# Kernel tuning notes

Hardware: AMD Instinct MI355X
Metric: run time of the kernel (lower is better)

## Reference

```python
import jax, jax.numpy as jnp
import numpy as np

N_STATIONS = 276
CONTEXT_LEN = 384  # args.context_len * 2
TARGET_LEN = 96
BATCH = 4096


def setup_inputs() -> dict:
    key = jax.random.key(0)
    k1, k2, k3, k4, k5, k6 = jax.random.split(key, 6)
    z = jax.random.normal(k1, (BATCH, CONTEXT_LEN), dtype=jnp.float32)
    stations = jax.random.randint(k2, (BATCH,), 0, N_STATIONS, dtype=jnp.int64)
    # per-station Linear params (nn.Linear(context_len, target_len) x n_stations)
    lim = 1.0 / np.sqrt(CONTEXT_LEN)
    W = jax.random.uniform(k3, (N_STATIONS, TARGET_LEN, CONTEXT_LEN), jnp.float32, -lim, lim)
    b = jax.random.uniform(k4, (N_STATIONS, TARGET_LEN), jnp.float32, -lim, lim)
    loc = jax.random.normal(k5, (N_STATIONS,), dtype=jnp.float32)
    scale = jax.random.uniform(k6, (N_STATIONS,), jnp.float32, 0.5, 2.0)
    return {"z": z, "stations": stations, "W": W, "b": b, "loc": loc, "scale": scale}


def reference(z, stations, W, b, loc, scale):
    # norm: (z - loc[i]) / scale[i]
    loc_i = loc[stations][:, None]      # (bs, 1)
    scale_i = scale[stations][:, None]  # (bs, 1)
    zn = (z - loc_i) / scale_i          # (bs, context_len)
    # per-sample station-specific Linear: batched GEMV via gathered weights
    out = jnp.einsum("boi,bi->bo", W[stations], zn) + b[stations]  # (bs, target_len)
    # denorm then softplus
    out = out * scale_i + loc_i
    return jax.nn.softplus(out)
```

## Files before the change

### kernel.cpp

```cpp
#include <hip/hip_runtime.h>
#include <hip/hip_bf16.h>
#include <math.h>

#define N_STATIONS 276
#define CTX 384
#define TGT 96
#define BATCH 4096
#define NT_MAX 532
#define NTASK (NT_MAX * 6)
#define CPX (NTASK / 8)

typedef __attribute__((ext_vector_type(8))) short bf16x8;
typedef __attribute__((ext_vector_type(4))) float f32x4;

__device__ __forceinline__ short f2bf(float f) {
    return (short)__builtin_bit_cast(unsigned short, __float2bfloat16(f));
}
__device__ __forceinline__ float bf2f(short h) {
    unsigned u = ((unsigned)(unsigned short)h) << 16;
    return __builtin_bit_cast(float, u);
}
__device__ __forceinline__ void cvt_hilo(float4 a, float4 b, bf16x8& hi, bf16x8& lo) {
    float f[8] = {a.x, a.y, a.z, a.w, b.x, b.y, b.z, b.w};
#pragma unroll
    for (int i = 0; i < 8; ++i) {
        short h = f2bf(f[i]);
        hi[i] = h;
        lo[i] = f2bf(f[i] - bf2f(h));
    }
}
__device__ __forceinline__ bf16x8 cvt_norm(float4 a, float4 b, float inv, float nb) {
    float f[8] = {a.x, a.y, a.z, a.w, b.x, b.y, b.z, b.w};
    bf16x8 r;
#pragma unroll
    for (int i = 0; i < 8; ++i) r[i] = f2bf(fmaf(f[i], inv, nb));
    return r;
}

__global__ __launch_bounds__(1024) void build_lists(
    const int* __restrict__ stations, int* __restrict__ ws)
{
    __shared__ int cnt[N_STATIONS], cnt2[N_STATIONS];
    __shared__ int poff[N_STATIONS + 1], tpoff[N_STATIONS + 1];
    const int tid = threadIdx.x;
    for (int i = tid; i < N_STATIONS; i += 1024) { cnt[i] = 0; cnt2[i] = 0; }
    __syncthreads();
    for (int b = tid; b < BATCH; b += 1024) atomicAdd(&cnt[stations[b]], 1);
    __syncthreads();
    if (tid < 64) {
        int run = 0, trun = 0;
        for (int base = 0; base < N_STATIONS; base += 64) {
            const int i = base + tid;
            int c  = (i < N_STATIONS) ? cnt[i] : 0;
            int v  = c, tv = (c + 15) >> 4;
#pragma unroll
            for (int off = 1; off < 64; off <<= 1) {
                int u  = __shfl_up(v, off, 64);
                int tu = __shfl_up(tv, off, 64);
                if (tid >= off) { v += u; tv += tu; }
            }
            if (i < N_STATIONS) { poff[i + 1] = run + v; tpoff[i + 1] = trun + tv; }
            run  += __shfl(v, 63, 64);
            trun += __shfl(tv, 63, 64);
        }
        if (tid == 0) { poff[0] = 0; tpoff[0] = 0; }
    }
    __syncthreads();
    int* order = ws + 1024;
    for (int b = tid; b < BATCH; b += 1024) {
        int s = stations[b];
        int p = atomicAdd(&cnt2[s], 1);
        order[poff[s] + p] = b;
    }
    for (int i = tid; i < N_STATIONS; i += 1024) {
        int n = (cnt[i] + 15) >> 4, base = tpoff[i];
        for (int t = 0; t < n; ++t) ws[1 + base + t] = (i << 16) | t;
    }
    if (tid <= N_STATIONS) ws[5120 + tid] = poff[tid];
    if (tid == 0) ws[0] = tpoff[N_STATIONS];
}

__global__ __launch_bounds__(64, 4) void nlinear_wave(
    const float* __restrict__ z,
    const float* __restrict__ W,
    const float* __restrict__ bias,
    const float* __restrict__ loc,
    const float* __restrict__ scale,
    const int*   __restrict__ ws,
    float*       __restrict__ out)
{
    const int ntasks = ws[0] * 6;
    const int b0 = blockIdx.x;
    const int b  = (b0 & 7) * CPX + (b0 >> 3);
    if (b >= ntasks) return;

    const int tile = b / 6;
    const int nt   = b - tile * 6;

    const int* tiles   = ws + 1;
    const int* order   = ws + 1024;
    const int* offsets = ws + 5120;

    const int pk = tiles[tile];
    const int s  = pk >> 16;
    const int tt = pk & 0xFFFF;
    const int start = offsets[s];
    const int m     = offsets[s + 1] - start;

    const int l  = threadIdx.x;
    const int lr = l & 15;
    const int kh = (l >> 4) * 8;

    const float lc = loc[s], sc = scale[s];
    const float inv = 1.0f / sc, nb = -lc * inv;

    int j = tt * 16 + lr; if (j > m - 1) j = m - 1;
    const float* zr = z + (size_t)order[start + j] * CTX + kh;
    bf16x8 af[12];
#pragma unroll
    for (int kk = 0; kk < 12; ++kk) {
        float4 a0 = *(const float4*)(zr + kk * 32);
        float4 a1 = *(const float4*)(zr + kk * 32 + 4);
        af[kk] = cvt_norm(a0, a1, inv, nb);
    }

    const float* wr = W + ((size_t)s * TGT + nt * 16 + lr) * CTX + kh;
    float4 wc0 = *(const float4*)(wr);
    float4 wc1 = *(const float4*)(wr + 4);
    float4 wc2 = *(const float4*)(wr + 32);
    float4 wc3 = *(const float4*)(wr + 36);

    f32x4 ah = {0.f, 0.f, 0.f, 0.f};
    f32x4 al = {0.f, 0.f, 0.f, 0.f};

#pragma unroll
    for (int i = 0; i < 6; ++i) {
        float4 wn0, wn1, wn2, wn3;
        if (i < 5) {
            const float* wnx = wr + (2 * i + 2) * 32;
            wn0 = *(const float4*)(wnx);
            wn1 = *(const float4*)(wnx + 4);
            wn2 = *(const float4*)(wnx + 32);
            wn3 = *(const float4*)(wnx + 36);
        }
        bf16x8 bhi, blo;
        cvt_hilo(wc0, wc1, bhi, blo);
        ah = __builtin_amdgcn_mfma_f32_16x16x32_bf16(af[2 * i], bhi, ah, 0, 0, 0);
        al = __builtin_amdgcn_mfma_f32_16x16x32_bf16(af[2 * i], blo, al, 0, 0, 0);
        cvt_hilo(wc2, wc3, bhi, blo);
        ah = __builtin_amdgcn_mfma_f32_16x16x32_bf16(af[2 * i + 1], bhi, ah, 0, 0, 0);
        al = __builtin_amdgcn_mfma_f32_16x16x32_bf16(af[2 * i + 1], blo, al, 0, 0, 0);
        if (i < 5) { wc0 = wn0; wc1 = wn1; wc2 = wn2; wc3 = wn3; }
    }

    const float bv = bias[(size_t)s * TGT + nt * 16 + lr];
    const int rbase = (l >> 4) * 4;
#pragma unroll
    for (int r = 0; r < 4; ++r) {
        const int jj = tt * 16 + rbase + r;
        if (jj < m) {
            const int oid = order[start + jj];
            float v = (ah[r] + al[r] + bv) * sc + lc;
            out[(size_t)oid * TGT + nt * 16 + lr] =
                fmaxf(v, 0.f) + log1pf(expf(-fabsf(v)));
        }
    }
}

extern "C" void kernel_launch(void* const* d_in, const int* in_sizes, int n_in,
                              void* d_out, int out_size, void* d_ws, size_t ws_size,
                              hipStream_t stream) {
    const float* z        = (const float*)d_in[0];
    const int*   stations = (const int*)  d_in[1];
    const float* W        = (const float*)d_in[2];
    const float* bias     = (const float*)d_in[3];
    const float* loc      = (const float*)d_in[4];
    const float* scale    = (const float*)d_in[5];
    float* out = (float*)d_out;
    int* ws = (int*)d_ws;

    build_lists<<<1, 1024, 0, stream>>>(stations, ws);
    nlinear_wave<<<NTASK, 64, 0, stream>>>(z, W, bias, loc, scale, ws, out);
}
```

Baseline: 31.84 us.

## Pre-stage normalized bf16 z tiles and drop hi/lo weight split

Adds a zstage kernel that gathers and normalizes the z rows for each station tile once, writes them to workspace as bf16 in MFMA fragment order, and stores per-tile metadata (station, row count, output indices). The main kernel no longer re-gathers and converts z for each of its six N-tiles. It also drops the hi/lo bf16 split of the weights, halving the MFMA count but reducing weight precision to plain bf16. The cost is an extra kernel launch, a workspace round-trip for z, and a possible accuracy loss.

New measurement: 30.88 us (median of 2 runs). 1.03x faster.

```diff
diff --git a/kernel.cpp b/kernel.cpp
--- a/kernel.cpp
+++ b/kernel.cpp
@@ -10,31 +10,14 @@
 #define NTASK (NT_MAX * 6)
 #define CPX (NTASK / 8)
 
+#define META_OFF 8192
+#define ZF_OFF   262144
+
 typedef __attribute__((ext_vector_type(8))) short bf16x8;
 typedef __attribute__((ext_vector_type(4))) float f32x4;
 
 __device__ __forceinline__ short f2bf(float f) {
     return (short)__builtin_bit_cast(unsigned short, __float2bfloat16(f));
-}
-__device__ __forceinline__ float bf2f(short h) {
-    unsigned u = ((unsigned)(unsigned short)h) << 16;
-    return __builtin_bit_cast(float, u);
-}
-__device__ __forceinline__ void cvt_hilo(float4 a, float4 b, bf16x8& hi, bf16x8& lo) {
-    float f[8] = {a.x, a.y, a.z, a.w, b.x, b.y, b.z, b.w};
-#pragma unroll
-    for (int i = 0; i < 8; ++i) {
-        short h = f2bf(f[i]);
-        hi[i] = h;
-        lo[i] = f2bf(f[i] - bf2f(h));
-    }
-}
-__device__ __forceinline__ bf16x8 cvt_norm(float4 a, float4 b, float inv, float nb) {
-    float f[8] = {a.x, a.y, a.z, a.w, b.x, b.y, b.z, b.w};
-    bf16x8 r;
-#pragma unroll
-    for (int i = 0; i < 8; ++i) r[i] = f2bf(fmaf(f[i], inv, nb));
-    return r;
 }
 
 __global__ __launch_bounds__(1024) void build_lists(
@@ -80,8 +63,53 @@
     if (tid == 0) ws[0] = tpoff[N_STATIONS];
 }
 
-__global__ __launch_bounds__(64, 4) void nlinear_wave(
+__global__ __launch_bounds__(256) void zstage(
     const float* __restrict__ z,
+    const float* __restrict__ loc,
+    const float* __restrict__ scale,
+    int* __restrict__ ws)
+{
+    const int ntiles = ws[0];
+    const int tb = blockIdx.x;
+    if (tb >= ntiles) return;
+
+    const int pk = ws[1 + tb];
+    const int s  = pk >> 16;
+    const int tt = pk & 0xFFFF;
+    const int* order   = ws + 1024;
+    const int* offsets = ws + 5120;
+    const int start = offsets[s];
+    const int m     = offsets[s + 1] - start;
+
+    const float lc = loc[s], inv = 1.0f / scale[s], nb = -lc * inv;
+
+    int* rec = ws + META_OFF + tb * 32;
+    const int t = threadIdx.x;
+    if (t < 16) {
+        int j = tt * 16 + t; if (j > m - 1) j = m - 1;
+        rec[2 + t] = order[start + j];
+    }
+    if (t == 0) { rec[0] = s; int mr = m - tt * 16; rec[1] = mr > 16 ? 16 : mr; }
+
+    unsigned short* zt = (unsigned short*)(ws + ZF_OFF) + (size_t)tb * 6144;
+    for (int q = t; q < 768; q += 256) {
+        const int kstep = q >> 6, lane = q & 63;
+        const int sample = lane & 15;
+        const int kb = kstep * 32 + (lane >> 4) * 8;
+        int j = tt * 16 + sample; if (j > m - 1) j = m - 1;
+        const float* zr = z + (size_t)order[start + j] * CTX + kb;
+        float4 a0 = *(const float4*)zr;
+        float4 a1 = *(const float4*)(zr + 4);
+        float f[8] = {a0.x, a0.y, a0.z, a0.w, a1.x, a1.y, a1.z, a1.w};
+        union { unsigned short u[8]; uint4 v; } o;
+#pragma unroll
+        for (int i = 0; i < 8; ++i)
+            o.u[i] = (unsigned short)f2bf(fmaf(f[i], inv, nb));
+        *(uint4*)(zt + (size_t)q * 8) = o.v;
+    }
+}
+
+__global__ __launch_bounds__(64, 4) void nlinear_hot(
     const float* __restrict__ W,
     const float* __restrict__ bias,
     const float* __restrict__ loc,
@@ -97,70 +125,48 @@
     const int tile = b / 6;
     const int nt   = b - tile * 6;
 
-    const int* tiles   = ws + 1;
-    const int* order   = ws + 1024;
-    const int* offsets = ws + 5120;
-
-    const int pk = tiles[tile];
-    const int s  = pk >> 16;
-    const int tt = pk & 0xFFFF;
-    const int start = offsets[s];
-    const int m     = offsets[s + 1] - start;
+    const int* rec = ws + META_OFF + tile * 32;
+    const int s    = rec[0];
+    const int mrem = rec[1];
 
     const int l  = threadIdx.x;
     const int lr = l & 15;
     const int kh = (l >> 4) * 8;
 
-    const float lc = loc[s], sc = scale[s];
-    const float inv = 1.0f / sc, nb = -lc * inv;
+    const float* wr = W + ((size_t)s * TGT + nt * 16 + lr) * CTX + kh;
+    const unsigned short* zt = (const unsigned short*)(ws + ZF_OFF) + (size_t)tile * 6144;
 
-    int j = tt * 16 + lr; if (j > m - 1) j = m - 1;
-    const float* zr = z + (size_t)order[start + j] * CTX + kh;
-    bf16x8 af[12];
+    f32x4 acc = {0.f, 0.f, 0.f, 0.f};
+    float4 wc0 = *(const float4*)(wr);
+    float4 wc1 = *(const float4*)(wr + 4);
+    bf16x8 za  = *(const bf16x8*)(zt + (size_t)l * 8);
+
 #pragma unroll
     for (int kk = 0; kk < 12; ++kk) {
-        float4 a0 = *(const float4*)(zr + kk * 32);
-        float4 a1 = *(const float4*)(zr + kk * 32 + 4);
-        af[kk] = cvt_norm(a0, a1, inv, nb);
+        float4 wn0, wn1; bf16x8 zn_;
+        if (kk < 11) {
+            wn0 = *(const float4*)(wr + (kk + 1) * 32);
+            wn1 = *(const float4*)(wr + (kk + 1) * 32 + 4);
+            zn_ = *(const bf16x8*)(zt + ((size_t)(kk + 1) * 64 + l) * 8);
+        }
+        bf16x8 bh;
+        bh[0] = f2bf(wc0.x); bh[1] = f2bf(wc0.y);
+        bh[2] = f2bf(wc0.z); bh[3] = f2bf(wc0.w);
+        bh[4] = f2bf(wc1.x); bh[5] = f2bf(wc1.y);
+        bh[6] = f2bf(wc1.z); bh[7] = f2bf(wc1.w);
+        acc = __builtin_amdgcn_mfma_f32_16x16x32_bf16(za, bh, acc, 0, 0, 0);
+        if (kk < 11) { wc0 = wn0; wc1 = wn1; za = zn_; }
     }
 
-    const float* wr = W + ((size_t)s * TGT + nt * 16 + lr) * CTX + kh;
-    float4 wc0 = *(const float4*)(wr);
-    float4 wc1 = *(const float4*)(wr + 4);
-    float4 wc2 = *(const float4*)(wr + 32);
-    float4 wc3 = *(const float4*)(wr + 36);
-
-    f32x4 ah = {0.f, 0.f, 0.f, 0.f};
-    f32x4 al = {0.f, 0.f, 0.f, 0.f};
-
-#pragma unroll
-    for (int i = 0; i < 6; ++i) {
-        float4 wn0, wn1, wn2, wn3;
-        if (i < 5) {
-            const float* wnx = wr + (2 * i + 2) * 32;
-            wn0 = *(const float4*)(wnx);
-            wn1 = *(const float4*)(wnx + 4);
-            wn2 = *(const float4*)(wnx + 32);
-            wn3 = *(const float4*)(wnx + 36);
-        }
-        bf16x8 bhi, blo;
-        cvt_hilo(wc0, wc1, bhi, blo);
-        ah = __builtin_amdgcn_mfma_f32_16x16x32_bf16(af[2 * i], bhi, ah, 0, 0, 0);
-        al = __builtin_amdgcn_mfma_f32_16x16x32_bf16(af[2 * i], blo, al, 0, 0, 0);
-        cvt_hilo(wc2, wc3, bhi, blo);
-        ah = __builtin_amdgcn_mfma_f32_16x16x32_bf16(af[2 * i + 1], bhi, ah, 0, 0, 0);
-        al = __builtin_amdgcn_mfma_f32_16x16x32_bf16(af[2 * i + 1], blo, al, 0, 0, 0);
-        if (i < 5) { wc0 = wn0; wc1 = wn1; wc2 = wn2; wc3 = wn3; }
-    }
-
+    const float sc = scale[s], lc = loc[s];
     const float bv = bias[(size_t)s * TGT + nt * 16 + lr];
     const int rbase = (l >> 4) * 4;
 #pragma unroll
     for (int r = 0; r < 4; ++r) {
-        const int jj = tt * 16 + rbase + r;
-        if (jj < m) {
-            const int oid = order[start + jj];
-            float v = (ah[r] + al[r] + bv) * sc + lc;
+        const int jj = rbase + r;
+        if (jj < mrem) {
+            const int oid = rec[2 + jj];
+            float v = (acc[r] + bv) * sc + lc;
             out[(size_t)oid * TGT + nt * 16 + lr] =
                 fmaxf(v, 0.f) + log1pf(expf(-fabsf(v)));
         }
@@ -180,5 +186,6 @@
     int* ws = (int*)d_ws;
 
     build_lists<<<1, 1024, 0, stream>>>(stations, ws);
-    nlinear_wave<<<NTASK, 64, 0, stream>>>(z, W, bias, loc, scale, ws, out);
+    zstage<<<NT_MAX, 256, 0, stream>>>(z, loc, scale, ws);
+    nlinear_hot<<<NTASK, 64, 0, stream>>>(W, bias, loc, scale, ws, out);
 }
```
